# Optimization experiments

Hardware: AMD Instinct MI355X
Metric: run time of the kernel (lower is better)

The kernel has to match this reference:

```python
import math
import jax, jax.numpy as jnp
import numpy as np

B, D, H, W, K = 32, 256, 64, 64, 6
CTX = 256
TEMP = 0.5
EPS_LN = 1e-5


def _layernorm(x, g, b):
    mu = x.mean(-1, keepdims=True)
    var = ((x - mu) ** 2).mean(-1, keepdims=True)
    return (x - mu) * jax.lax.rsqrt(var + EPS_LN) * g + b


def _linear(x, w, b):
    return x @ w.T + b


def _gru_cell(x, h, wih, bih, whh, bhh):
    gi = x @ wih.T + bih
    gh = h @ whh.T + bhh
    i_r, i_z, i_n = jnp.split(gi, 3, axis=-1)
    h_r, h_z, h_n = jnp.split(gh, 3, axis=-1)
    r = jax.nn.sigmoid(i_r + h_r)
    z = jax.nn.sigmoid(i_z + h_z)
    n = jnp.tanh(i_n + r * h_n)
    return (1.0 - z) * n + z * h


def setup_inputs() -> dict:
    key = jax.random.key(0)
    ks = jax.random.split(key, 24)
    s = 0.05
    p = {
        'features': jax.random.normal(ks[0], (B, D, H, W), jnp.float32),
        'task_context': jax.random.normal(ks[1], (B, CTX), jnp.float32),
        'ctx_w1': jax.random.normal(ks[2], (D, CTX), jnp.float32) * s,
        'ctx_b1': jnp.zeros((D,), jnp.float32),
        'ctx_w2': jax.random.normal(ks[3], (K * D, D), jnp.float32) * s,
        'ctx_b2': jnp.zeros((K * D,), jnp.float32),
        'q_w': jax.random.normal(ks[4], (D, D), jnp.float32) * s,
        'q_b': jnp.zeros((D,), jnp.float32),
        'k_w': jax.random.normal(ks[5], (D, D), jnp.float32) * s,
        'k_b': jnp.zeros((D,), jnp.float32),
        'v_w': jax.random.normal(ks[6], (D, D), jnp.float32) * s,
        'v_b': jnp.zeros((D,), jnp.float32),
        'qn_g': jnp.ones((D,), jnp.float32),
        'qn_b': jnp.zeros((D,), jnp.float32),
        'fn_g': jnp.ones((D,), jnp.float32),
        'fn_b': jnp.zeros((D,), jnp.float32),
        'stop_w1': jax.random.normal(ks[7], (D // 2, D + 1), jnp.float32) * s,
        'stop_b1': jnp.zeros((D // 2,), jnp.float32),
        'stop_w2': jax.random.normal(ks[8], (1, D // 2), jnp.float32) * s,
        'stop_b2': jnp.zeros((1,), jnp.float32),
        'gru_wih': jax.random.normal(ks[9], (3 * D, D), jnp.float32) * s,
        'gru_bih': jnp.zeros((3 * D,), jnp.float32),
        'gru_whh': jax.random.normal(ks[10], (3 * D, D), jnp.float32) * s,
        'gru_bhh': jnp.zeros((3 * D,), jnp.float32),
    }
    return p


def _forward(features, task_context, ctx_w1, ctx_b1, ctx_w2, ctx_b2,
             q_w, q_b, k_w, k_b, v_w, v_b, qn_g, qn_b, fn_g, fn_b,
             stop_w1, stop_b1, stop_w2, stop_b2,
             gru_wih, gru_bih, gru_whh, gru_bhh):
    scale = math.sqrt(D)
    N = H * W
    # task-conditioned clue queries: (B, K, D), clamped
    h1 = jax.nn.gelu(_linear(task_context, ctx_w1, ctx_b1), approximate=False)
    clue_queries = _linear(h1, ctx_w2, ctx_b2).reshape(B, K, D)
    clue_queries = jnp.clip(clue_queries, -10.0, 10.0)

    # (B, N, D), normalized; k/v projections are loop-invariant -> hoist
    feats = jnp.transpose(features, (0, 2, 3, 1)).reshape(B, N, D)
    feats = _layernorm(feats, fn_g, fn_b)
    kp = _linear(feats, k_w, k_b)  # (B, N, D)
    vp = _linear(feats, v_w, v_b)  # (B, N, D)

    rows = jnp.repeat(jnp.arange(H, dtype=jnp.float32), W)  # (N,)
    cols = jnp.tile(jnp.arange(W, dtype=jnp.float32), H)    # (N,)
    max_entropy = math.log(N + 1e-6)

    def step(carry, qk):
        query_state, cum_mask = carry  # (B,D), (B,N)
        query = _layernorm(qk + query_state, qn_g, qn_b)
        q = _linear(query, q_w, q_b)  # (B, D)
        scores = jnp.einsum('bd,bnd->bn', q, kp) / scale
        scores = scores + jnp.log(jnp.clip(cum_mask, 1e-6))
        scores = jnp.clip(scores, -50.0, 50.0)
        logits = jnp.clip(scores / max(TEMP, 1e-10), -50.0, 50.0)
        attn = jnp.clip(jax.nn.softmax(logits, axis=-1), 1e-8)  # (B, N)
        row_c = attn @ rows
        col_c = attn @ cols
        centroid = jnp.stack([row_c, col_c], axis=-1)  # (B, 2)
        attended = jnp.einsum('bn,bnd->bd', attn, vp)  # (B, D)
        new_state = _gru_cell(attended, query_state, gru_wih, gru_bih, gru_whh, gru_bhh)
        a = jnp.clip(attn, 1e-6)
        entropy = -(a * jnp.log(a)).sum(-1, keepdims=True) / max_entropy
        s1 = jax.nn.gelu(_linear(jnp.concatenate([attended, entropy], -1), stop_w1, stop_b1), approximate=False)
        stop_raw = _linear(s1, stop_w2, stop_b2)[:, 0]
        stop = 4.0 * jnp.tanh(stop_raw / 4.0)
        new_mask = jnp.clip(cum_mask * (1.0 - 0.9 * jax.lax.stop_gradient(attn)), 1e-6)
        return (new_state, new_mask), (centroid, attn.reshape(B, H, W), stop)

    init = (jnp.zeros((B, D), jnp.float32), jnp.ones((B, N), jnp.float32))
    qks = jnp.transpose(clue_queries, (1, 0, 2))  # (K, B, D)
    _, (cents, attns, stops) = jax.lax.scan(step, init, qks)
    centroids = jnp.transpose(cents, (1, 0, 2))        # (B, K, 2)
    attention_maps = jnp.transpose(attns, (1, 0, 2, 3))  # (B, K, H, W)
    stop_logits = jnp.transpose(stops, (1, 0))          # (B, K)
    return centroids, attention_maps, stop_logits


def reference(features, task_context, ctx_w1, ctx_b1, ctx_w2, ctx_b2,
              q_w, q_b, k_w, k_b, v_w, v_b, qn_g, qn_b, fn_g, fn_b,
              stop_w1, stop_b1, stop_w2, stop_b2,
              gru_wih, gru_bih, gru_whh, gru_bhh):
    return _forward(features, task_context, ctx_w1, ctx_b1, ctx_w2, ctx_b2,
                    q_w, q_b, k_w, k_b, v_w, v_b, qn_g, qn_b, fn_g, fn_b,
                    stop_w1, stop_b1, stop_w2, stop_b2,
                    gru_wih, gru_bih, gru_whh, gru_bhh)
```

## Files before the change

kernel.cpp:

```cpp
#include <hip/hip_runtime.h>
#include <hip/hip_bf16.h>

#define NB 32
#define ND 256
#define NN_ 4096
#define NK 6

typedef short bf16x8 __attribute__((ext_vector_type(8)));
typedef float f32x4 __attribute__((ext_vector_type(4)));

__device__ __forceinline__ float bf2f(unsigned int u) {
    union { unsigned int i; float f; } v; v.i = (u & 0xffffu) << 16; return v.f;
}
__device__ __forceinline__ unsigned short f2bf(float f) {
    __hip_bfloat16 h = __float2bfloat16(f);
    return *reinterpret_cast<unsigned short*>(&h);
}
__device__ __forceinline__ float gelu_exact(float x) {
    return 0.5f * x * (1.0f + erff(x * 0.70710678118654752f));
}

__global__ void k_prep(const float* __restrict__ kw, const float* __restrict__ vw,
                       unsigned short* __restrict__ kwb, unsigned short* __restrict__ vwb,
                       float* __restrict__ mask, float* __restrict__ accs) {
    int i = blockIdx.x * 256 + threadIdx.x;
    if (i < 65536) kwb[i] = f2bf(kw[i]);
    else if (i < 131072) vwb[i - 65536] = f2bf(vw[i - 65536]);
    else if (i < 262144) mask[i - 131072] = 1.f;
    else if (i < 262912) accs[i - 262144] = 0.f;
}

__global__ void k_ctx(const float* __restrict__ tc, const float* __restrict__ w1,
                      const float* __restrict__ b1, const float* __restrict__ w2,
                      const float* __restrict__ b2, float* __restrict__ clue) {
    int b = blockIdx.x, t = threadIdx.x;
    __shared__ __align__(16) float tcs[256];
    __shared__ __align__(16) float h1[256];
    tcs[t] = tc[b * 256 + t];
    __syncthreads();
    const float4* wr = (const float4*)(w1 + (size_t)t * 256);
    const float4* xs = (const float4*)tcs;
    float acc = b1[t];
#pragma unroll 8
    for (int i = 0; i < 64; ++i) {
        float4 w = wr[i], x = xs[i];
        acc += w.x * x.x + w.y * x.y + w.z * x.z + w.w * x.w;
    }
    h1[t] = gelu_exact(acc);
    __syncthreads();
    const float4* hs = (const float4*)h1;
    for (int r = 0; r < 6; ++r) {
        int row = r * 256 + t;
        const float4* w2r = (const float4*)(w2 + (size_t)row * 256);
        float a2 = b2[row];
#pragma unroll 8
        for (int i = 0; i < 64; ++i) {
            float4 w = w2r[i], x = hs[i];
            a2 += w.x * x.x + w.y * x.y + w.z * x.z + w.w * x.w;
        }
        clue[b * 1536 + row] = fminf(fmaxf(a2, -10.f), 10.f);
    }
}

__global__ __launch_bounds__(256, 4) void k_kv(
    const float* __restrict__ features, const float* __restrict__ fn_g,
    const float* __restrict__ fn_b, const unsigned short* __restrict__ kwb,
    const unsigned short* __restrict__ vwb, const float* __restrict__ kb,
    const float* __restrict__ vb, unsigned short* __restrict__ kp,
    unsigned short* __restrict__ vp) {
    int tile = blockIdx.x, b = blockIdx.y;
    int n0 = tile * 64;
    int t = threadIdx.x;

    __shared__ __align__(16) unsigned short A[64][264];

    int dd = t & 15, nq = t >> 4;
    const float* fb = features + (size_t)b * 1048576 + n0 + nq * 4;
    unsigned int pk[8][4];
    float s[4] = {0, 0, 0, 0}, s2[4] = {0, 0, 0, 0};
#pragma unroll
    for (int p = 0; p < 8; ++p) {
        int d0 = p * 32 + dd * 2;
        float4 a0 = *reinterpret_cast<const float4*>(fb + (size_t)d0 * 4096);
        float4 a1 = *reinterpret_cast<const float4*>(fb + (size_t)(d0 + 1) * 4096);
        s[0] += a0.x + a1.x; s2[0] += a0.x * a0.x + a1.x * a1.x;
        s[1] += a0.y + a1.y; s2[1] += a0.y * a0.y + a1.y * a1.y;
        s[2] += a0.z + a1.z; s2[2] += a0.z * a0.z + a1.z * a1.z;
        s[3] += a0.w + a1.w; s2[3] += a0.w * a0.w + a1.w * a1.w;
        pk[p][0] = (unsigned int)f2bf(a0.x) | ((unsigned int)f2bf(a1.x) << 16);
        pk[p][1] = (unsigned int)f2bf(a0.y) | ((unsigned int)f2bf(a1.y) << 16);
        pk[p][2] = (unsigned int)f2bf(a0.z) | ((unsigned int)f2bf(a1.z) << 16);
        pk[p][3] = (unsigned int)f2bf(a0.w) | ((unsigned int)f2bf(a1.w) << 16);
    }
#pragma unroll
    for (int m = 1; m < 16; m <<= 1) {
#pragma unroll
        for (int k = 0; k < 4; ++k) {
            s[k] += __shfl_xor(s[k], m, 64);
            s2[k] += __shfl_xor(s2[k], m, 64);
        }
    }
    float mm[4], rr[4];
#pragma unroll
    for (int k = 0; k < 4; ++k) {
        float mean = s[k] * (1.f / 256.f);
        float var = s2[k] * (1.f / 256.f) - mean * mean;
        mm[k] = mean; rr[k] = rsqrtf(var + 1e-5f);
    }
#pragma unroll
    for (int p = 0; p < 8; ++p) {
        int d0 = p * 32 + dd * 2;
        float g0 = fn_g[d0], g1 = fn_g[d0 + 1];
        float e0 = fn_b[d0], e1 = fn_b[d0 + 1];
#pragma unroll
        for (int k = 0; k < 4; ++k) {
            float x0 = bf2f(pk[p][k]);
            float x1 = bf2f(pk[p][k] >> 16);
            unsigned int lo = f2bf((x0 - mm[k]) * rr[k] * g0 + e0);
            unsigned int hi = f2bf((x1 - mm[k]) * rr[k] * g1 + e1);
            *reinterpret_cast<unsigned int*>(&A[nq * 4 + k][d0]) = lo | (hi << 16);
        }
    }
    __syncthreads();

    int lane = t & 63, wv = t >> 6;
    int r = lane & 15, qd = lane >> 4;
#pragma unroll
    for (int mat = 0; mat < 2; ++mat) {
        const unsigned short* wb = mat ? vwb : kwb;
        const float* bias = mat ? vb : kb;
        unsigned short* outp = mat ? vp : kp;
#pragma unroll
        for (int dtl = 0; dtl < 4; ++dtl) {
            int dt = wv * 4 + dtl;
            const unsigned short* wrow = wb + (size_t)(dt * 16 + r) * 256 + qd * 8;
            f32x4 acc0 = {0, 0, 0, 0}, acc1 = {0, 0, 0, 0};
            f32x4 acc2 = {0, 0, 0, 0}, acc3 = {0, 0, 0, 0};
#pragma unroll
            for (int ks = 0; ks < 8; ++ks) {
                bf16x8 af = *reinterpret_cast<const bf16x8*>(wrow + ks * 32);
                int col = ks * 32 + qd * 8;
                bf16x8 b0 = *reinterpret_cast<const bf16x8*>(&A[r][col]);
                bf16x8 b1 = *reinterpret_cast<const bf16x8*>(&A[16 + r][col]);
                bf16x8 b2 = *reinterpret_cast<const bf16x8*>(&A[32 + r][col]);
                bf16x8 b3 = *reinterpret_cast<const bf16x8*>(&A[48 + r][col]);
                acc0 = __builtin_amdgcn_mfma_f32_16x16x32_bf16(af, b0, acc0, 0, 0, 0);
                acc1 = __builtin_amdgcn_mfma_f32_16x16x32_bf16(af, b1, acc1, 0, 0, 0);
                acc2 = __builtin_amdgcn_mfma_f32_16x16x32_bf16(af, b2, acc2, 0, 0, 0);
                acc3 = __builtin_amdgcn_mfma_f32_16x16x32_bf16(af, b3, acc3, 0, 0, 0);
            }
            int dbase = dt * 16 + qd * 4;
            float b0_ = bias[dbase], b1_ = bias[dbase + 1];
            float b2_ = bias[dbase + 2], b3_ = bias[dbase + 3];
            f32x4 aa[4] = {acc0, acc1, acc2, acc3};
#pragma unroll
            for (int nt = 0; nt < 4; ++nt) {
                int n_g = n0 + nt * 16 + r;
                unsigned int lo = ((unsigned int)f2bf(aa[nt][1] + b1_) << 16) | (unsigned int)f2bf(aa[nt][0] + b0_);
                unsigned int hi = ((unsigned int)f2bf(aa[nt][3] + b3_) << 16) | (unsigned int)f2bf(aa[nt][2] + b2_);
                uint2 o = make_uint2(lo, hi);
                *reinterpret_cast<uint2*>(outp + ((size_t)(b * 4096 + n_g)) * 256 + dbase) = o;
            }
        }
    }
}

__global__ __launch_bounds__(256, 4) void k_qscore(
    const float* __restrict__ clue, const float* __restrict__ gacc,
    const float* __restrict__ state_prev, float* __restrict__ state_cur,
    const float* __restrict__ qn_g, const float* __restrict__ qn_b,
    const float* __restrict__ q_w, const float* __restrict__ q_b,
    const unsigned short* __restrict__ kp, const float* __restrict__ mask,
    float* __restrict__ escore, float* __restrict__ accs,
    float* __restrict__ attended, int kstep) {
    int c = blockIdx.x, b = blockIdx.y, t = threadIdx.x;
    int lane = t & 63, wv = t >> 6;
    __shared__ __align__(16) float qs[256];
    __shared__ float sred[8];
    float h = 0.f;
    if (kstep > 0) {
        float sr = gacc[(b * 4 + 0) * 256 + t];
        float sz = gacc[(b * 4 + 1) * 256 + t];
        float gin = gacc[(b * 4 + 2) * 256 + t];
        float ghn = gacc[(b * 4 + 3) * 256 + t];
        float r = 1.f / (1.f + expf(-sr));
        float z = 1.f / (1.f + expf(-sz));
        float nv = tanhf(gin + r * ghn);
        h = (1.f - z) * nv + z * state_prev[b * 256 + t];
    }
    if (c == 0) {
        state_cur[b * 256 + t] = h;
        attended[b * 256 + t] = 0.f;
    }
    float x = clue[(b * 6 + kstep) * 256 + t] + h;
    float s = x, s2 = x * x;
#pragma unroll
    for (int off = 32; off > 0; off >>= 1) {
        s += __shfl_down(s, off, 64);
        s2 += __shfl_down(s2, off, 64);
    }
    if (lane == 0) { sred[wv] = s; sred[4 + wv] = s2; }
    __syncthreads();
    float muv = (sred[0] + sred[1] + sred[2] + sred[3]) * (1.f / 256.f);
    float var = (sred[4] + sred[5] + sred[6] + sred[7]) * (1.f / 256.f) - muv * muv;
    float rs = rsqrtf(var + 1e-5f);
    qs[t] = (x - muv) * rs * qn_g[t] + qn_b[t];
    __syncthreads();
    const float4* wr = (const float4*)(q_w + (size_t)t * 256);
    const float4* xs4 = (const float4*)qs;
    float qv = q_b[t];
#pragma unroll 8
    for (int i = 0; i < 64; ++i) {
        float4 w = wr[i], xx = xs4[i];
        qv += w.x * xx.x + w.y * xx.y + w.z * xx.z + w.w * xx.w;
    }
    __syncthreads();
    qs[t] = qv;
    __syncthreads();
    int l = t & 7, rg = t >> 3;
    float dsum = 0.f;
#pragma unroll
    for (int pp = 0; pp < 8; ++pp) {
        int n = c * 256 + pp * 32 + rg;
        const uint4* kr = reinterpret_cast<const uint4*>(kp + ((size_t)(b * 4096 + n)) * 256 + l * 8);
        float dot = 0.f;
#pragma unroll
        for (int j = 0; j < 4; ++j) {
            uint4 rv = kr[j * 8];
            const float* qq = qs + j * 64 + l * 8;
            dot += bf2f(rv.x) * qq[0] + bf2f(rv.x >> 16) * qq[1]
                 + bf2f(rv.y) * qq[2] + bf2f(rv.y >> 16) * qq[3]
                 + bf2f(rv.z) * qq[4] + bf2f(rv.z >> 16) * qq[5]
                 + bf2f(rv.w) * qq[6] + bf2f(rv.w >> 16) * qq[7];
        }
        dot += __shfl_xor(dot, 1, 64);
        dot += __shfl_xor(dot, 2, 64);
        dot += __shfl_xor(dot, 4, 64);
        float sc = dot * 0.0625f + logf(mask[(size_t)b * 4096 + n]);
        sc = fminf(fmaxf(sc, -50.f), 50.f);
        float lg = fminf(fmaxf(sc * 2.f, -50.f), 50.f);
        float e = expf(lg);
        if (l == 0) escore[(size_t)b * 4096 + n] = e;
        dsum += e;
    }
    dsum *= 0.125f;
#pragma unroll
    for (int off = 32; off > 0; off >>= 1) dsum += __shfl_down(dsum, off, 64);
    if (lane == 0) sred[wv] = dsum;
    __syncthreads();
    if (t == 0) atomicAdd(&accs[kstep * 128 + b], sred[0] + sred[1] + sred[2] + sred[3]);
}

__global__ __launch_bounds__(256, 4) void k_attn2(
    const float* __restrict__ escore, const unsigned short* __restrict__ vp,
    float* __restrict__ mask, float* __restrict__ accs,
    float* __restrict__ attended, float* __restrict__ out_amap, int kstep) {
    int c = blockIdx.x, b = blockIdx.y, t = threadIdx.x;
    int n0 = c * 256, n = n0 + t;
    int lane = t & 63, wv = t >> 6;
    __shared__ float ash[256];
    __shared__ __align__(16) float part[8][264];
    __shared__ float sred[12];
    float denom = accs[kstep * 128 + b];
    float a = fmaxf(escore[(size_t)b * 4096 + n] / denom, 1e-8f);
    out_amap[((size_t)(b * 6 + kstep)) * 4096 + n] = a;
    ash[t] = a;
    float rw = (float)(n >> 6), cl = (float)(n & 63);
    float ac = fmaxf(a, 1e-6f);
    float al = ac * logf(ac);
    float s0 = a * rw, s1 = a * cl, s2 = al;
#pragma unroll
    for (int off = 32; off > 0; off >>= 1) {
        s0 += __shfl_down(s0, off, 64);
        s1 += __shfl_down(s1, off, 64);
        s2 += __shfl_down(s2, off, 64);
    }
    if (lane == 0) { sred[wv] = s0; sred[4 + wv] = s1; sred[8 + wv] = s2; }
    float mv = mask[(size_t)b * 4096 + n] * (1.f - 0.9f * a);
    mask[(size_t)b * 4096 + n] = fmaxf(mv, 1e-6f);
    __syncthreads();
    if (t == 0) {
        atomicAdd(&accs[kstep * 128 + 32 + b], sred[0] + sred[1] + sred[2] + sred[3]);
        atomicAdd(&accs[kstep * 128 + 64 + b], sred[4] + sred[5] + sred[6] + sred[7]);
        atomicAdd(&accs[kstep * 128 + 96 + b], sred[8] + sred[9] + sred[10] + sred[11]);
    }
    int dbase = (t & 31) * 8, noff = t >> 5;
    const unsigned short* vb = vp + ((size_t)(b * 4096 + n0 + noff * 32)) * 256 + dbase;
    float a0 = 0, a1 = 0, a2 = 0, a3 = 0, a4 = 0, a5 = 0, a6 = 0, a7 = 0;
#pragma unroll 4
    for (int j = 0; j < 32; ++j) {
        uint4 rv = *reinterpret_cast<const uint4*>(vb + (size_t)j * 256);
        float w = ash[noff * 32 + j];
        a0 += w * bf2f(rv.x); a1 += w * bf2f(rv.x >> 16);
        a2 += w * bf2f(rv.y); a3 += w * bf2f(rv.y >> 16);
        a4 += w * bf2f(rv.z); a5 += w * bf2f(rv.z >> 16);
        a6 += w * bf2f(rv.w); a7 += w * bf2f(rv.w >> 16);
    }
    *reinterpret_cast<float4*>(&part[noff][dbase])     = make_float4(a0, a1, a2, a3);
    *reinterpret_cast<float4*>(&part[noff][dbase + 4]) = make_float4(a4, a5, a6, a7);
    __syncthreads();
    float sum = part[0][t] + part[1][t] + part[2][t] + part[3][t]
              + part[4][t] + part[5][t] + part[6][t] + part[7][t];
    atomicAdd(&attended[b * 256 + t], sum);
}

__global__ __launch_bounds__(256, 2) void k_gate(
    const float* __restrict__ attended, const float* __restrict__ state_cur,
    const float* __restrict__ wih, const float* __restrict__ bih,
    const float* __restrict__ whh, const float* __restrict__ bhh,
    const float* __restrict__ sw1, const float* __restrict__ sb1,
    const float* __restrict__ sw2, const float* __restrict__ sb2,
    const float* __restrict__ accs, float* __restrict__ gacc,
    float* __restrict__ out_cent, float* __restrict__ out_stop, int kstep) {
    int bb = blockIdx.x, t = threadIdx.x;
    int lane = t & 63, wv = t >> 6;
    __shared__ __align__(16) float att[256];
    __shared__ __align__(16) float st[256];
    __shared__ float sred[4];
    if (bb < 96) {
        if (kstep == 5) return;
        int b = bb & 31, g = bb >> 5;
        att[t] = attended[b * 256 + t];
        st[t] = state_cur[b * 256 + t];
        __syncthreads();
        int row = g * 256 + t;
        const float4* wi = (const float4*)(wih + (size_t)row * 256);
        const float4* wh = (const float4*)(whh + (size_t)row * 256);
        const float4* av = (const float4*)att;
        const float4* sv = (const float4*)st;
        float ai = bih[row], ah = bhh[row];
#pragma unroll 4
        for (int i = 0; i < 64; ++i) {
            float4 w1 = wi[i], x1 = av[i];
            ai += w1.x * x1.x + w1.y * x1.y + w1.z * x1.z + w1.w * x1.w;
            float4 w2 = wh[i], x2 = sv[i];
            ah += w2.x * x2.x + w2.y * x2.y + w2.z * x2.z + w2.w * x2.w;
        }
        if (g == 2) {
            gacc[(b * 4 + 2) * 256 + t] = ai;
            gacc[(b * 4 + 3) * 256 + t] = ah;
        } else {
            gacc[(b * 4 + g) * 256 + t] = ai + ah;
        }
    } else {
        int b = bb - 96;
        att[t] = attended[b * 256 + t];
        __syncthreads();
        float entv = -accs[kstep * 128 + 96 + b] * 0.12022458674074826f;
        float v = 0.f;
        if (t < 128) {
            const float* wr = sw1 + (size_t)t * 257;
            float acc = sb1[t];
#pragma unroll 8
            for (int i = 0; i < 256; ++i) acc += att[i] * wr[i];
            acc += entv * wr[256];
            v = gelu_exact(acc) * sw2[t];
        }
#pragma unroll
        for (int off = 32; off > 0; off >>= 1) v += __shfl_down(v, off, 64);
        if (lane == 0) sred[wv] = v;
        __syncthreads();
        if (t == 0) {
            float sraw = sb2[0] + sred[0] + sred[1] + sred[2] + sred[3];
            out_stop[b * 6 + kstep] = 4.f * tanhf(sraw * 0.25f);
            out_cent[(b * 6 + kstep) * 2 + 0] = accs[kstep * 128 + 32 + b];
            out_cent[(b * 6 + kstep) * 2 + 1] = accs[kstep * 128 + 64 + b];
        }
    }
}

extern "C" void kernel_launch(void* const* d_in, const int* in_sizes, int n_in,
                              void* d_out, int out_size, void* d_ws, size_t ws_size,
                              hipStream_t stream) {
    const float* features     = (const float*)d_in[0];
    const float* task_context = (const float*)d_in[1];
    const float* ctx_w1 = (const float*)d_in[2];
    const float* ctx_b1 = (const float*)d_in[3];
    const float* ctx_w2 = (const float*)d_in[4];
    const float* ctx_b2 = (const float*)d_in[5];
    const float* q_w = (const float*)d_in[6];
    const float* q_b = (const float*)d_in[7];
    const float* k_w = (const float*)d_in[8];
    const float* k_b = (const float*)d_in[9];
    const float* v_w = (const float*)d_in[10];
    const float* v_b = (const float*)d_in[11];
    const float* qn_g = (const float*)d_in[12];
    const float* qn_b = (const float*)d_in[13];
    const float* fn_g = (const float*)d_in[14];
    const float* fn_b = (const float*)d_in[15];
    const float* stop_w1 = (const float*)d_in[16];
    const float* stop_b1 = (const float*)d_in[17];
    const float* stop_w2 = (const float*)d_in[18];
    const float* stop_b2 = (const float*)d_in[19];
    const float* gru_wih = (const float*)d_in[20];
    const float* gru_bih = (const float*)d_in[21];
    const float* gru_whh = (const float*)d_in[22];
    const float* gru_bhh = (const float*)d_in[23];

    unsigned short* kwb = (unsigned short*)d_ws;
    unsigned short* vwb = kwb + 65536;
    unsigned short* kp  = vwb + 65536;
    unsigned short* vp  = kp + (size_t)NB * NN_ * ND;
    float* clue     = (float*)(vp + (size_t)NB * NN_ * ND);
    float* state0   = clue + NB * NK * ND;
    float* state1   = state0 + NB * ND;
    float* attended = state1 + NB * ND;
    float* mask     = attended + NB * ND;
    float* escore   = mask + NB * NN_;
    float* accs     = escore + NB * NN_;
    float* gacc     = accs + NK * 4 * NB;

    float* out_cent = (float*)d_out;
    float* out_amap = out_cent + NB * NK * 2;
    float* out_stop = out_amap + (size_t)NB * NK * NN_;

    float* stbuf[2] = {state0, state1};

    k_prep<<<1027, 256, 0, stream>>>(k_w, v_w, kwb, vwb, mask, accs);
    k_ctx<<<32, 256, 0, stream>>>(task_context, ctx_w1, ctx_b1, ctx_w2, ctx_b2, clue);
    k_kv<<<dim3(64, 32), 256, 0, stream>>>(features, fn_g, fn_b, kwb, vwb, k_b, v_b, kp, vp);
    for (int k = 0; k < NK; ++k) {
        float* scur = stbuf[k & 1];
        float* sprev = stbuf[1 - (k & 1)];
        k_qscore<<<dim3(16, 32), 256, 0, stream>>>(clue, gacc, sprev, scur, qn_g, qn_b,
                                                   q_w, q_b, kp, mask, escore, accs, attended, k);
        k_attn2<<<dim3(16, 32), 256, 0, stream>>>(escore, vp, mask, accs, attended, out_amap, k);
        k_gate<<<128, 256, 0, stream>>>(attended, scur, gru_wih, gru_bih, gru_whh, gru_bhh,
                                        stop_w1, stop_b1, stop_w2, stop_b2, accs, gacc,
                                        out_cent, out_stop, k);
    }
}
```

Baseline: 750.2 us.

## Fuse unnormalized value accumulation into score kernel and defer softmax normalization

The e*V accumulation moves from the attention kernel into the score kernel, using the unnormalized exp scores held in shared memory. The result is divided by the softmax denominator later, in the gate kernel, which removes the extra pass that re-read the scores before touching V and lets the lighter attention-map and mask kernel run vectorized over fewer blocks. Double-buffered accumulators let the next step clear the other buffer. The prep and context kernels are merged into one launch, and the K/V projection loop is reordered to reuse B fragments across matrices. The score kernel now carries more shared memory and work, which may lower occupancy.

```diff
diff --git a/kernel.cpp b/kernel.cpp
--- a/kernel.cpp
+++ b/kernel.cpp
@@ -20,22 +20,26 @@
     return 0.5f * x * (1.0f + erff(x * 0.70710678118654752f));
 }
 
-__global__ void k_prep(const float* __restrict__ kw, const float* __restrict__ vw,
-                       unsigned short* __restrict__ kwb, unsigned short* __restrict__ vwb,
-                       float* __restrict__ mask, float* __restrict__ accs) {
-    int i = blockIdx.x * 256 + threadIdx.x;
-    if (i < 65536) kwb[i] = f2bf(kw[i]);
-    else if (i < 131072) vwb[i - 65536] = f2bf(vw[i - 65536]);
-    else if (i < 262144) mask[i - 131072] = 1.f;
-    else if (i < 262912) accs[i - 262144] = 0.f;
-}
-
-__global__ void k_ctx(const float* __restrict__ tc, const float* __restrict__ w1,
-                      const float* __restrict__ b1, const float* __restrict__ w2,
-                      const float* __restrict__ b2, float* __restrict__ clue) {
-    int b = blockIdx.x, t = threadIdx.x;
+__global__ void k_setup(const float* __restrict__ kw, const float* __restrict__ vw,
+                        unsigned short* __restrict__ kwb, unsigned short* __restrict__ vwb,
+                        float* __restrict__ mask, float* __restrict__ accs,
+                        float* __restrict__ sumev0,
+                        const float* __restrict__ tc, const float* __restrict__ w1,
+                        const float* __restrict__ b1, const float* __restrict__ w2,
+                        const float* __restrict__ b2, float* __restrict__ clue) {
     __shared__ __align__(16) float tcs[256];
     __shared__ __align__(16) float h1[256];
+    int blk = blockIdx.x, t = threadIdx.x;
+    if (blk < 1059) {
+        int i = blk * 256 + t;
+        if (i < 65536) kwb[i] = f2bf(kw[i]);
+        else if (i < 131072) vwb[i - 65536] = f2bf(vw[i - 65536]);
+        else if (i < 262144) mask[i - 131072] = 1.f;
+        else if (i < 262912) accs[i - 262144] = 0.f;
+        else if (i < 271104) sumev0[i - 262912] = 0.f;
+        return;
+    }
+    int b = blk - 1059;
     tcs[t] = tc[b * 256 + t];
     __syncthreads();
     const float4* wr = (const float4*)(w1 + (size_t)t * 256);
@@ -126,40 +130,34 @@
     int lane = t & 63, wv = t >> 6;
     int r = lane & 15, qd = lane >> 4;
 #pragma unroll
-    for (int mat = 0; mat < 2; ++mat) {
-        const unsigned short* wb = mat ? vwb : kwb;
-        const float* bias = mat ? vb : kb;
-        unsigned short* outp = mat ? vp : kp;
-#pragma unroll
-        for (int dtl = 0; dtl < 4; ++dtl) {
-            int dt = wv * 4 + dtl;
-            const unsigned short* wrow = wb + (size_t)(dt * 16 + r) * 256 + qd * 8;
-            f32x4 acc0 = {0, 0, 0, 0}, acc1 = {0, 0, 0, 0};
-            f32x4 acc2 = {0, 0, 0, 0}, acc3 = {0, 0, 0, 0};
-#pragma unroll
-            for (int ks = 0; ks < 8; ++ks) {
-                bf16x8 af = *reinterpret_cast<const bf16x8*>(wrow + ks * 32);
-                int col = ks * 32 + qd * 8;
-                bf16x8 b0 = *reinterpret_cast<const bf16x8*>(&A[r][col]);
-                bf16x8 b1 = *reinterpret_cast<const bf16x8*>(&A[16 + r][col]);
-                bf16x8 b2 = *reinterpret_cast<const bf16x8*>(&A[32 + r][col]);
-                bf16x8 b3 = *reinterpret_cast<const bf16x8*>(&A[48 + r][col]);
-                acc0 = __builtin_amdgcn_mfma_f32_16x16x32_bf16(af, b0, acc0, 0, 0, 0);
-                acc1 = __builtin_amdgcn_mfma_f32_16x16x32_bf16(af, b1, acc1, 0, 0, 0);
-                acc2 = __builtin_amdgcn_mfma_f32_16x16x32_bf16(af, b2, acc2, 0, 0, 0);
-                acc3 = __builtin_amdgcn_mfma_f32_16x16x32_bf16(af, b3, acc3, 0, 0, 0);
-            }
-            int dbase = dt * 16 + qd * 4;
-            float b0_ = bias[dbase], b1_ = bias[dbase + 1];
-            float b2_ = bias[dbase + 2], b3_ = bias[dbase + 3];
-            f32x4 aa[4] = {acc0, acc1, acc2, acc3};
-#pragma unroll
-            for (int nt = 0; nt < 4; ++nt) {
+    for (int nt = 0; nt < 4; ++nt) {
+        bf16x8 bfrag[8];
+#pragma unroll
+        for (int ks = 0; ks < 8; ++ks)
+            bfrag[ks] = *reinterpret_cast<const bf16x8*>(&A[nt * 16 + r][ks * 32 + qd * 8]);
+#pragma unroll
+        for (int mat = 0; mat < 2; ++mat) {
+            const unsigned short* wb = mat ? vwb : kwb;
+            const float* bias = mat ? vb : kb;
+            unsigned short* outp = mat ? vp : kp;
+#pragma unroll
+            for (int dtl = 0; dtl < 4; ++dtl) {
+                int dt = wv * 4 + dtl;
+                const unsigned short* wrow = wb + (size_t)(dt * 16 + r) * 256 + qd * 8;
+                f32x4 acc = {0.f, 0.f, 0.f, 0.f};
+#pragma unroll
+                for (int ks = 0; ks < 8; ++ks) {
+                    bf16x8 af = *reinterpret_cast<const bf16x8*>(wrow + ks * 32);
+                    acc = __builtin_amdgcn_mfma_f32_16x16x32_bf16(af, bfrag[ks], acc, 0, 0, 0);
+                }
+                int dbase = dt * 16 + qd * 4;
+                unsigned int lo = ((unsigned int)f2bf(acc[1] + bias[dbase + 1]) << 16)
+                                | (unsigned int)f2bf(acc[0] + bias[dbase]);
+                unsigned int hi = ((unsigned int)f2bf(acc[3] + bias[dbase + 3]) << 16)
+                                | (unsigned int)f2bf(acc[2] + bias[dbase + 2]);
                 int n_g = n0 + nt * 16 + r;
-                unsigned int lo = ((unsigned int)f2bf(aa[nt][1] + b1_) << 16) | (unsigned int)f2bf(aa[nt][0] + b0_);
-                unsigned int hi = ((unsigned int)f2bf(aa[nt][3] + b3_) << 16) | (unsigned int)f2bf(aa[nt][2] + b2_);
-                uint2 o = make_uint2(lo, hi);
-                *reinterpret_cast<uint2*>(outp + ((size_t)(b * 4096 + n_g)) * 256 + dbase) = o;
+                *reinterpret_cast<uint2*>(outp + ((size_t)(b * 4096 + n_g)) * 256 + dbase)
+                    = make_uint2(lo, hi);
             }
         }
     }
@@ -170,12 +168,15 @@
     const float* __restrict__ state_prev, float* __restrict__ state_cur,
     const float* __restrict__ qn_g, const float* __restrict__ qn_b,
     const float* __restrict__ q_w, const float* __restrict__ q_b,
-    const unsigned short* __restrict__ kp, const float* __restrict__ mask,
-    float* __restrict__ escore, float* __restrict__ accs,
-    float* __restrict__ attended, int kstep) {
+    const unsigned short* __restrict__ kp, const unsigned short* __restrict__ vp,
+    const float* __restrict__ mask, float* __restrict__ escore,
+    float* __restrict__ accs, float* __restrict__ sumev,
+    float* __restrict__ sumev_other, int kstep) {
     int c = blockIdx.x, b = blockIdx.y, t = threadIdx.x;
     int lane = t & 63, wv = t >> 6;
     __shared__ __align__(16) float qs[256];
+    __shared__ float ash[256];
+    __shared__ __align__(16) float part[8][264];
     __shared__ float sred[8];
     float h = 0.f;
     if (kstep > 0) {
@@ -190,7 +191,7 @@
     }
     if (c == 0) {
         state_cur[b * 256 + t] = h;
-        attended[b * 256 + t] = 0.f;
+        sumev_other[b * 256 + t] = 0.f;
     }
     float x = clue[(b * 6 + kstep) * 256 + t] + h;
     float s = x, s2 = x * x;
@@ -221,7 +222,8 @@
     float dsum = 0.f;
 #pragma unroll
     for (int pp = 0; pp < 8; ++pp) {
-        int n = c * 256 + pp * 32 + rg;
+        int nl = pp * 32 + rg;
+        int n = c * 256 + nl;
         const uint4* kr = reinterpret_cast<const uint4*>(kp + ((size_t)(b * 4096 + n)) * 256 + l * 8);
         float dot = 0.f;
 #pragma unroll
@@ -240,7 +242,10 @@
         sc = fminf(fmaxf(sc, -50.f), 50.f);
         float lg = fminf(fmaxf(sc * 2.f, -50.f), 50.f);
         float e = expf(lg);
-        if (l == 0) escore[(size_t)b * 4096 + n] = e;
+        if (l == 0) {
+            escore[(size_t)b * 4096 + n] = e;
+            ash[nl] = e;
+        }
         dsum += e;
     }
     dsum *= 0.125f;
@@ -249,43 +254,8 @@
     if (lane == 0) sred[wv] = dsum;
     __syncthreads();
     if (t == 0) atomicAdd(&accs[kstep * 128 + b], sred[0] + sred[1] + sred[2] + sred[3]);
-}
-
-__global__ __launch_bounds__(256, 4) void k_attn2(
-    const float* __restrict__ escore, const unsigned short* __restrict__ vp,
-    float* __restrict__ mask, float* __restrict__ accs,
-    float* __restrict__ attended, float* __restrict__ out_amap, int kstep) {
-    int c = blockIdx.x, b = blockIdx.y, t = threadIdx.x;
-    int n0 = c * 256, n = n0 + t;
-    int lane = t & 63, wv = t >> 6;
-    __shared__ float ash[256];
-    __shared__ __align__(16) float part[8][264];
-    __shared__ float sred[12];
-    float denom = accs[kstep * 128 + b];
-    float a = fmaxf(escore[(size_t)b * 4096 + n] / denom, 1e-8f);
-    out_amap[((size_t)(b * 6 + kstep)) * 4096 + n] = a;
-    ash[t] = a;
-    float rw = (float)(n >> 6), cl = (float)(n & 63);
-    float ac = fmaxf(a, 1e-6f);
-    float al = ac * logf(ac);
-    float s0 = a * rw, s1 = a * cl, s2 = al;
-#pragma unroll
-    for (int off = 32; off > 0; off >>= 1) {
-        s0 += __shfl_down(s0, off, 64);
-        s1 += __shfl_down(s1, off, 64);
-        s2 += __shfl_down(s2, off, 64);
-    }
-    if (lane == 0) { sred[wv] = s0; sred[4 + wv] = s1; sred[8 + wv] = s2; }
-    float mv = mask[(size_t)b * 4096 + n] * (1.f - 0.9f * a);
-    mask[(size_t)b * 4096 + n] = fmaxf(mv, 1e-6f);
-    __syncthreads();
-    if (t == 0) {
-        atomicAdd(&accs[kstep * 128 + 32 + b], sred[0] + sred[1] + sred[2] + sred[3]);
-        atomicAdd(&accs[kstep * 128 + 64 + b], sred[4] + sred[5] + sred[6] + sred[7]);
-        atomicAdd(&accs[kstep * 128 + 96 + b], sred[8] + sred[9] + sred[10] + sred[11]);
-    }
     int dbase = (t & 31) * 8, noff = t >> 5;
-    const unsigned short* vb = vp + ((size_t)(b * 4096 + n0 + noff * 32)) * 256 + dbase;
+    const unsigned short* vb = vp + ((size_t)(b * 4096 + c * 256 + noff * 32)) * 256 + dbase;
     float a0 = 0, a1 = 0, a2 = 0, a3 = 0, a4 = 0, a5 = 0, a6 = 0, a7 = 0;
 #pragma unroll 4
     for (int j = 0; j < 32; ++j) {
@@ -301,11 +271,53 @@
     __syncthreads();
     float sum = part[0][t] + part[1][t] + part[2][t] + part[3][t]
               + part[4][t] + part[5][t] + part[6][t] + part[7][t];
-    atomicAdd(&attended[b * 256 + t], sum);
+    atomicAdd(&sumev[b * 256 + t], sum);
+}
+
+__global__ __launch_bounds__(256, 4) void k_attn2(
+    const float* __restrict__ escore, float* __restrict__ mask,
+    float* __restrict__ accs, float* __restrict__ out_amap, int kstep) {
+    int c = blockIdx.x, b = blockIdx.y, t = threadIdx.x;
+    int lane = t & 63, wv = t >> 6;
+    __shared__ float sred[12];
+    int n4 = (c * 256 + t) * 4;
+    float inv = 1.f / accs[kstep * 128 + b];
+    float4 e4 = *reinterpret_cast<const float4*>(&escore[(size_t)b * 4096 + n4]);
+    float4 m4 = *reinterpret_cast<const float4*>(&mask[(size_t)b * 4096 + n4]);
+    float a[4] = {fmaxf(e4.x * inv, 1e-8f), fmaxf(e4.y * inv, 1e-8f),
+                  fmaxf(e4.z * inv, 1e-8f), fmaxf(e4.w * inv, 1e-8f)};
+    *reinterpret_cast<float4*>(&out_amap[((size_t)(b * 6 + kstep)) * 4096 + n4])
+        = make_float4(a[0], a[1], a[2], a[3]);
+    float mv[4] = {m4.x, m4.y, m4.z, m4.w};
+    float s0 = 0.f, s1 = 0.f, s2 = 0.f;
+#pragma unroll
+    for (int j = 0; j < 4; ++j) {
+        int n = n4 + j;
+        s0 += a[j] * (float)(n >> 6);
+        s1 += a[j] * (float)(n & 63);
+        float ac = fmaxf(a[j], 1e-6f);
+        s2 += ac * logf(ac);
+        mv[j] = fmaxf(mv[j] * (1.f - 0.9f * a[j]), 1e-6f);
+    }
+    *reinterpret_cast<float4*>(&mask[(size_t)b * 4096 + n4])
+        = make_float4(mv[0], mv[1], mv[2], mv[3]);
+#pragma unroll
+    for (int off = 32; off > 0; off >>= 1) {
+        s0 += __shfl_down(s0, off, 64);
+        s1 += __shfl_down(s1, off, 64);
+        s2 += __shfl_down(s2, off, 64);
+    }
+    if (lane == 0) { sred[wv] = s0; sred[4 + wv] = s1; sred[8 + wv] = s2; }
+    __syncthreads();
+    if (t == 0) {
+        atomicAdd(&accs[kstep * 128 + 32 + b], sred[0] + sred[1] + sred[2] + sred[3]);
+        atomicAdd(&accs[kstep * 128 + 64 + b], sred[4] + sred[5] + sred[6] + sred[7]);
+        atomicAdd(&accs[kstep * 128 + 96 + b], sred[8] + sred[9] + sred[10] + sred[11]);
+    }
 }
 
 __global__ __launch_bounds__(256, 2) void k_gate(
-    const float* __restrict__ attended, const float* __restrict__ state_cur,
+    const float* __restrict__ sumev, const float* __restrict__ state_cur,
     const float* __restrict__ wih, const float* __restrict__ bih,
     const float* __restrict__ whh, const float* __restrict__ bhh,
     const float* __restrict__ sw1, const float* __restrict__ sb1,
@@ -320,7 +332,8 @@
     if (bb < 96) {
         if (kstep == 5) return;
         int b = bb & 31, g = bb >> 5;
-        att[t] = attended[b * 256 + t];
+        float inv = 1.f / accs[kstep * 128 + b];
+        att[t] = sumev[b * 256 + t] * inv;
         st[t] = state_cur[b * 256 + t];
         __syncthreads();
         int row = g * 256 + t;
@@ -344,7 +357,8 @@
         }
     } else {
         int b = bb - 96;
-        att[t] = attended[b * 256 + t];
+        float inv = 1.f / accs[kstep * 128 + b];
+        att[t] = sumev[b * 256 + t] * inv;
         __syncthreads();
         float entv = -accs[kstep * 128 + 96 + b] * 0.12022458674074826f;
         float v = 0.f;
@@ -404,8 +418,9 @@
     float* clue     = (float*)(vp + (size_t)NB * NN_ * ND);
     float* state0   = clue + NB * NK * ND;
     float* state1   = state0 + NB * ND;
-    float* attended = state1 + NB * ND;
-    float* mask     = attended + NB * ND;
+    float* sumev0   = state1 + NB * ND;
+    float* sumev1   = sumev0 + NB * ND;
+    float* mask     = sumev1 + NB * ND;
     float* escore   = mask + NB * NN_;
     float* accs     = escore + NB * NN_;
     float* gacc     = accs + NK * 4 * NB;
@@ -415,17 +430,21 @@
     float* out_stop = out_amap + (size_t)NB * NK * NN_;
 
     float* stbuf[2] = {state0, state1};
-
-    k_prep<<<1027, 256, 0, stream>>>(k_w, v_w, kwb, vwb, mask, accs);
-    k_ctx<<<32, 256, 0, stream>>>(task_context, ctx_w1, ctx_b1, ctx_w2, ctx_b2, clue);
+    float* evbuf[2] = {sumev0, sumev1};
+
+    k_setup<<<1091, 256, 0, stream>>>(k_w, v_w, kwb, vwb, mask, accs, sumev0,
+                                      task_context, ctx_w1, ctx_b1, ctx_w2, ctx_b2, clue);
     k_kv<<<dim3(64, 32), 256, 0, stream>>>(features, fn_g, fn_b, kwb, vwb, k_b, v_b, kp, vp);
     for (int k = 0; k < NK; ++k) {
         float* scur = stbuf[k & 1];
         float* sprev = stbuf[1 - (k & 1)];
+        float* ev = evbuf[k & 1];
+        float* evo = evbuf[1 - (k & 1)];
         k_qscore<<<dim3(16, 32), 256, 0, stream>>>(clue, gacc, sprev, scur, qn_g, qn_b,
-                                                   q_w, q_b, kp, mask, escore, accs, attended, k);
-        k_attn2<<<dim3(16, 32), 256, 0, stream>>>(escore, vp, mask, accs, attended, out_amap, k);
-        k_gate<<<128, 256, 0, stream>>>(attended, scur, gru_wih, gru_bih, gru_whh, gru_bhh,
+                                                   q_w, q_b, kp, vp, mask, escore, accs,
+                                                   ev, evo, k);
+        k_attn2<<<dim3(4, 32), 256, 0, stream>>>(escore, mask, accs, out_amap, k);
+        k_gate<<<128, 256, 0, stream>>>(ev, scur, gru_wih, gru_bih, gru_whh, gru_bhh,
                                         stop_w1, stop_b1, stop_w2, stop_b2, accs, gacc,
                                         out_cent, out_stop, k);
     }
```

After: 901.5 us. +20.2%, slower.
